# Performance work log

Hardware: AMD Instinct MI355X
Metric: run time of the kernel (lower is better)

The kernel has to match this reference:

```python
import jax, jax.numpy as jnp
import numpy as np

N_DIM = 512
HIDDEN = 512


def setup_inputs() -> dict:
    key = jax.random.key(0)
    ks = jax.random.split(key, 9)
    s = 0.02
    x = jax.random.normal(ks[0], (4, 4096, N_DIM), dtype=jnp.float32)
    Wq = jax.random.normal(ks[1], (N_DIM, HIDDEN), dtype=jnp.float32) * s
    bq = jnp.zeros((HIDDEN,), dtype=jnp.float32)
    Wk = jax.random.normal(ks[2], (N_DIM, HIDDEN), dtype=jnp.float32) * s
    bk = jnp.zeros((HIDDEN,), dtype=jnp.float32)
    Wv = jax.random.normal(ks[3], (N_DIM, HIDDEN), dtype=jnp.float32) * s
    bv = jnp.zeros((HIDDEN,), dtype=jnp.float32)
    Wo = jax.random.normal(ks[4], (HIDDEN, N_DIM), dtype=jnp.float32) * s
    bo = jnp.zeros((N_DIM,), dtype=jnp.float32)
    return {"x": x, "Wq": Wq, "bq": bq, "Wk": Wk, "bk": bk,
            "Wv": Wv, "bv": bv, "Wo": Wo, "bo": bo}


def reference(x, Wq, bq, Wk, bk, Wv, bv, Wo, bo):
    # x: [B, S, n_dim]
    q = jnp.einsum('bsd,dh->bsh', x, Wq) + bq  # [B,S,H]
    k = jnp.einsum('bsd,dh->bsh', x, Wk) + bk
    v = jnp.einsum('bsd,dh->bsh', x, Wv) + bv
    # NOTE: original module uses UNSCALED scores (no 1/sqrt(d))
    scores = jnp.einsum('bqh,bkh->bqk', q, k)  # [B,S,S]
    attn = jax.nn.softmax(scores, axis=-1)
    y = jnp.einsum('bqk,bkh->bqh', attn, v)
    return jnp.einsum('bsh,hd->bsd', y, Wo) + bo
```

## Files before the change

### kernel.cpp

```cpp
#include <hip/hip_runtime.h>
#include <hip/hip_bf16.h>

typedef _Float16 h8 __attribute__((ext_vector_type(8)));
typedef __bf16   b8 __attribute__((ext_vector_type(8)));
typedef float    f4 __attribute__((ext_vector_type(4)));

#define B_    4
#define S_    4096
#define D_    512
#define ROWS_ (B_ * S_)
#define NQKV_ 1536
#define BR    64
#define BC2   64
#define NIT2  (S_ / BC2)
#define KP3   520
#define KT3   (BC2 * KP3)
#define PP3   72
#define MSH   (30.0f * 1.4426950408889634f)
#define L2E   1.4426950408889634f

__device__ __forceinline__ void gl_lds16(const void* src, void* dst) {
    __builtin_amdgcn_global_load_lds(
        (const __attribute__((address_space(1))) unsigned int*)src,
        (__attribute__((address_space(3))) unsigned int*)dst, 16, 0, 0);
}

__global__ __launch_bounds__(256) void convert_all(
    const float* __restrict__ x,
    const float* __restrict__ Wq, const float* __restrict__ Wk, const float* __restrict__ Wv,
    const float* __restrict__ bq, const float* __restrict__ bk, const float* __restrict__ bv,
    const float* __restrict__ Wo,
    _Float16* __restrict__ xh, _Float16* __restrict__ wqkvT, _Float16* __restrict__ woT,
    float* __restrict__ bqkv)
{
    long i0 = (long)blockIdx.x * blockDim.x + threadIdx.x;
    long stride = (long)gridDim.x * blockDim.x;
    const long NX  = (long)ROWS_ * D_;
    const long NW  = (long)D_ * NQKV_;
    const long NWO = (long)D_ * D_;

    for (long i = i0; i < NX; i += stride) xh[i] = (_Float16)x[i];

    for (long i = i0; i < NW; i += stride) {
        long n = i >> 9, k = i & 511;
        long which = n >> 9, nn = n & 511;
        const float* W = (which == 0) ? Wq : (which == 1) ? Wk : Wv;
        wqkvT[i] = (_Float16)W[k * 512 + nn];
    }
    for (long i = i0; i < NWO; i += stride) {
        long n = i >> 9, k = i & 511;
        woT[i] = (_Float16)Wo[k * 512 + n];
    }
    for (long i = i0; i < NQKV_; i += stride) {
        long which = i >> 9, nn = i & 511;
        const float* bb = (which == 0) ? bq : (which == 1) ? bk : bv;
        bqkv[i] = bb[nn];
    }
}

template <bool OUT_F16>
__global__ __launch_bounds__(256) void gemm_bt(
    const _Float16* __restrict__ A, const _Float16* __restrict__ BT,
    const float* __restrict__ bias, void* __restrict__ Cout,
    int M, int N, int K, __bf16* __restrict__ vPout)
{
    __shared__ _Float16 As[128 * 32];
    __shared__ _Float16 Bs[128 * 32];

    int tid = threadIdx.x;
    int w = tid >> 6, lane = tid & 63, quad = lane >> 4, l16 = lane & 15;
    long row0 = (long)blockIdx.x * 128, col0 = (long)blockIdx.y * 128;
    int wr = (w >> 1) * 64, wc = (w & 1) * 64;

    f4 acc[4][4];
    for (int i = 0; i < 4; i++)
        for (int j = 0; j < 4; j++) acc[i][j] = (f4){0.f, 0.f, 0.f, 0.f};

    const int lrow = lane >> 2;
    const int lcol = (lane & 3) * 8;

    for (int k0 = 0; k0 < K; k0 += 32) {
        __syncthreads();
#pragma unroll
        for (int i = 0; i < 2; i++) {
            int seg = w * 2 + i;
            gl_lds16(A  + (row0 + seg * 16 + lrow) * K + k0 + lcol, As + seg * 512);
            gl_lds16(BT + (col0 + seg * 16 + lrow) * K + k0 + lcol, Bs + seg * 512);
        }
        __syncthreads();
        h8 af[4], bf[4];
        for (int i = 0; i < 4; i++) af[i] = *(const h8*)(As + (wr + i * 16 + l16) * 32 + quad * 8);
        for (int j = 0; j < 4; j++) bf[j] = *(const h8*)(Bs + (wc + j * 16 + l16) * 32 + quad * 8);
        for (int i = 0; i < 4; i++)
            for (int j = 0; j < 4; j++)
                acc[i][j] = __builtin_amdgcn_mfma_f32_16x16x32_f16(af[i], bf[j], acc[i][j], 0, 0, 0);
    }

    if (OUT_F16 && vPout != nullptr && col0 >= 1024) {
        for (int i = 0; i < 4; i++) {
            long row = row0 + wr + i * 16 + quad * 4;
            int bb   = (int)(row >> 12);
            int s    = (int)(row & 4095);
            int kt32 = s >> 5;
            int qq   = (s >> 3) & 3;
            int k3   = s & 7;
            for (int j = 0; j < 4; j++) {
                int dglob = (int)(col0 - 1024) + wc + j * 16;
                int dt = dglob >> 4;
                long off = (((long)bb * 128 + kt32) * 32 + dt) * 512
                         + (qq * 16 + l16) * 8 + k3;
                union { __bf16 h[4]; uint2 u2; } pk;
                for (int r = 0; r < 4; r++)
                    pk.h[r] = (__bf16)(acc[i][j][r] + bias[col0 + wc + j * 16 + l16]);
                *(uint2*)(vPout + off) = pk.u2;
            }
        }
    } else {
        for (int i = 0; i < 4; i++)
            for (int j = 0; j < 4; j++)
                for (int r = 0; r < 4; r++) {
                    long row = row0 + wr + i * 16 + quad * 4 + r;
                    long col = col0 + wc + j * 16 + l16;
                    float v = acc[i][j][r] + bias[col];
                    if (OUT_F16) ((_Float16*)Cout)[row * N + col] = (_Float16)v;
                    else         ((float*)Cout)[row * N + col]    = v;
                }
    }
}

__global__ __launch_bounds__(512, 2) void attn_kernel(const _Float16* __restrict__ qkv,
                                                      const __bf16* __restrict__ vP,
                                                      _Float16* __restrict__ yb)
{
    __shared__ _Float16 Ks[2 * KT3];
    __shared__ __bf16   Ps[2 * BR * PP3];
    __shared__ float    lpart[2][BR];

    const int tid = threadIdx.x;
    const int w = tid >> 6, lane = tid & 63, quad = lane >> 4, l16 = lane & 15;

    const int bid = blockIdx.x;
    const int xcd = bid & 7;
    const int b = xcd >> 1;
    const long q0 = (long)((xcd & 1) * 32 + (bid >> 3)) * BR;
    const long rowBase = (long)b * S_;

    const _Float16* kbase = qkv + rowBase * NQKV_ + 512;

#pragma unroll
    for (int i = 0; i < 8; i++) {
        int r = w * 8 + i;
        gl_lds16(kbase + (long)r * NQKV_ + lane * 8, Ks + r * KP3);
    }

    if (w < 4) {
        const int rs0 = (w & 1) * 32;
        const int kg0 = (w >> 1) * 32;

        h8 Qf0[16], Qf1[16];
        {
            const _Float16* q0p = qkv + (rowBase + q0 + rs0 + l16) * NQKV_;
            const _Float16* q1p = q0p + 16 * NQKV_;
#pragma unroll
            for (int ks = 0; ks < 16; ks++) {
                Qf0[ks] = *(const h8*)(q0p + ks * 32 + quad * 8);
                Qf1[ks] = *(const h8*)(q1p + ks * 32 + quad * 8);
            }
        }
        float lo0[4] = {0.f, 0.f, 0.f, 0.f};
        float lo1[4] = {0.f, 0.f, 0.f, 0.f};

        __syncthreads();

        for (int kt = 0; kt < NIT2; kt++) {
            if (kt + 1 < NIT2) {
                const _Float16* kn = kbase + (long)(kt + 1) * BC2 * NQKV_;
                _Float16* kd = Ks + ((kt + 1) & 1) * KT3;
#pragma unroll
                for (int i = 0; i < 8; i++) {
                    int r = w * 8 + i;
                    gl_lds16(kn + (long)r * NQKV_ + lane * 8, kd + r * KP3);
                }
            }
            f4 S[2][2][2];
#pragma unroll
            for (int a = 0; a < 2; a++)
#pragma unroll
                for (int c = 0; c < 2; c++)
#pragma unroll
                    for (int d = 0; d < 2; d++) S[a][c][d] = (f4){0.f, 0.f, 0.f, 0.f};
            const _Float16* kr0 = Ks + (kt & 1) * KT3 + (kg0 + l16) * KP3 + quad * 8;
            const _Float16* kr1 = kr0 + 16 * KP3;
            __builtin_amdgcn_s_setprio(1);
#pragma unroll
            for (int ks = 0; ks < 8; ks++) {
                h8 a0 = *(const h8*)(kr0 + ks * 32);
                h8 a1 = *(const h8*)(kr0 + (ks + 8) * 32);
                h8 c0 = *(const h8*)(kr1 + ks * 32);
                h8 c1 = *(const h8*)(kr1 + (ks + 8) * 32);
                S[0][0][0] = __builtin_amdgcn_mfma_f32_16x16x32_f16(Qf0[ks],     a0, S[0][0][0], 0, 0, 0);
                S[1][0][0] = __builtin_amdgcn_mfma_f32_16x16x32_f16(Qf1[ks],     a0, S[1][0][0], 0, 0, 0);
                S[0][1][0] = __builtin_amdgcn_mfma_f32_16x16x32_f16(Qf0[ks],     c0, S[0][1][0], 0, 0, 0);
                S[1][1][0] = __builtin_amdgcn_mfma_f32_16x16x32_f16(Qf1[ks],     c0, S[1][1][0], 0, 0, 0);
                S[0][0][1] = __builtin_amdgcn_mfma_f32_16x16x32_f16(Qf0[ks + 8], a1, S[0][0][1], 0, 0, 0);
                S[1][0][1] = __builtin_amdgcn_mfma_f32_16x16x32_f16(Qf1[ks + 8], a1, S[1][0][1], 0, 0, 0);
                S[0][1][1] = __builtin_amdgcn_mfma_f32_16x16x32_f16(Qf0[ks + 8], c1, S[0][1][1], 0, 0, 0);
                S[1][1][1] = __builtin_amdgcn_mfma_f32_16x16x32_f16(Qf1[ks + 8], c1, S[1][1][1], 0, 0, 0);
            }
            __builtin_amdgcn_s_setprio(0);
            __bf16* ps = Ps + (kt & 1) * (BR * PP3);
#pragma unroll
            for (int r = 0; r < 4; r++) {
                float p00 = exp2f((S[0][0][0][r] + S[0][0][1][r]) * L2E - MSH);
                float p01 = exp2f((S[0][1][0][r] + S[0][1][1][r]) * L2E - MSH);
                float p10 = exp2f((S[1][0][0][r] + S[1][0][1][r]) * L2E - MSH);
                float p11 = exp2f((S[1][1][0][r] + S[1][1][1][r]) * L2E - MSH);
                __bf16 b00 = (__bf16)p00, b01 = (__bf16)p01;
                __bf16 b10 = (__bf16)p10, b11 = (__bf16)p11;
                int r0 = (rs0 + quad * 4 + r) * PP3;
                int r1 = (rs0 + 16 + quad * 4 + r) * PP3;
                ps[r0 + kg0 + l16]      = b00;
                ps[r0 + kg0 + 16 + l16] = b01;
                ps[r1 + kg0 + l16]      = b10;
                ps[r1 + kg0 + 16 + l16] = b11;
                lo0[r] += (float)b00 + (float)b01;
                lo1[r] += (float)b10 + (float)b11;
            }
            __builtin_amdgcn_sched_barrier(0);
            asm volatile("s_waitcnt vmcnt(0)");
            asm volatile("s_waitcnt lgkmcnt(0)");
            __builtin_amdgcn_s_barrier();
            __builtin_amdgcn_sched_barrier(0);
        }

#pragma unroll
        for (int r = 0; r < 4; r++)
#pragma unroll
            for (int m = 1; m < 16; m <<= 1) {
                lo0[r] += __shfl_xor(lo0[r], m, 16);
                lo1[r] += __shfl_xor(lo1[r], m, 16);
            }
        if (l16 == 0)
            for (int r = 0; r < 4; r++) {
                lpart[w >> 1][rs0 + quad * 4 + r]      = lo0[r];
                lpart[w >> 1][rs0 + 16 + quad * 4 + r] = lo1[r];
            }
        __syncthreads();
    } else {
        const int cv = w - 4;
        const __bf16* vpbase = vP + ((long)b * 128 * 32 + cv * 8) * 512 + lane * 8;

        f4 O[4][8];
#pragma unroll
        for (int rt = 0; rt < 4; rt++)
#pragma unroll
            for (int ct = 0; ct < 8; ct++) O[rt][ct] = (f4){0.f, 0.f, 0.f, 0.f};
        b8 vreg[16];

        __syncthreads();

        for (int kt = 0; kt < NIT2; kt++) {
            if (kt + 1 < NIT2) {
                const _Float16* kn = kbase + (long)(kt + 1) * BC2 * NQKV_;
                _Float16* kd = Ks + ((kt + 1) & 1) * KT3;
#pragma unroll
                for (int i = 0; i < 8; i++) {
                    int r = w * 8 + i;
                    gl_lds16(kn + (long)r * NQKV_ + lane * 8, kd + r * KP3);
                }
            }
            __builtin_amdgcn_sched_barrier(0);
            if (kt > 0) {
                if (kt < NIT2 - 1) asm volatile("s_waitcnt vmcnt(8)");
                else               asm volatile("s_waitcnt vmcnt(0)");
                const __bf16* ps = Ps + ((kt - 1) & 1) * (BR * PP3);
                __builtin_amdgcn_s_setprio(1);
#pragma unroll
                for (int rt = 0; rt < 4; rt++) {
                    b8 pa0 = *(const b8*)(ps + (rt * 16 + l16) * PP3 + quad * 8);
                    b8 pa1 = *(const b8*)(ps + (rt * 16 + l16) * PP3 + 32 + quad * 8);
#pragma unroll
                    for (int ct = 0; ct < 8; ct++) {
                        O[rt][ct] = __builtin_amdgcn_mfma_f32_16x16x32_bf16(pa0, vreg[ct],     O[rt][ct], 0, 0, 0);
                        O[rt][ct] = __builtin_amdgcn_mfma_f32_16x16x32_bf16(pa1, vreg[8 + ct], O[rt][ct], 0, 0, 0);
                    }
                }
                __builtin_amdgcn_s_setprio(0);
            }
            {
                const __bf16* vs0 = vpbase + (long)(2 * kt) * (32 * 512);
#pragma unroll
                for (int ct = 0; ct < 8; ct++) {
                    vreg[ct]     = *(const b8*)(vs0 + ct * 512);
                    vreg[8 + ct] = *(const b8*)(vs0 + 32 * 512 + ct * 512);
                }
            }
            __builtin_amdgcn_sched_barrier(0);
            asm volatile("s_waitcnt vmcnt(16)");
            asm volatile("s_waitcnt lgkmcnt(0)");
            __builtin_amdgcn_s_barrier();
            __builtin_amdgcn_sched_barrier(0);
        }
        asm volatile("s_waitcnt vmcnt(0)");
        {
            const __bf16* ps = Ps + ((NIT2 - 1) & 1) * (BR * PP3);
#pragma unroll
            for (int rt = 0; rt < 4; rt++) {
                b8 pa0 = *(const b8*)(ps + (rt * 16 + l16) * PP3 + quad * 8);
                b8 pa1 = *(const b8*)(ps + (rt * 16 + l16) * PP3 + 32 + quad * 8);
#pragma unroll
                for (int ct = 0; ct < 8; ct++) {
                    O[rt][ct] = __builtin_amdgcn_mfma_f32_16x16x32_bf16(pa0, vreg[ct],     O[rt][ct], 0, 0, 0);
                    O[rt][ct] = __builtin_amdgcn_mfma_f32_16x16x32_bf16(pa1, vreg[8 + ct], O[rt][ct], 0, 0, 0);
                }
            }
        }
        __syncthreads();

#pragma unroll
        for (int rt = 0; rt < 4; rt++) {
            f4 l0 = *(const f4*)(&lpart[0][rt * 16 + quad * 4]);
            f4 l1 = *(const f4*)(&lpart[1][rt * 16 + quad * 4]);
            float li[4];
            for (int r = 0; r < 4; r++) li[r] = 1.f / (l0[r] + l1[r]);
            for (int ct = 0; ct < 8; ct++)
                for (int r = 0; r < 4; r++) {
                    long row = rowBase + q0 + rt * 16 + quad * 4 + r;
                    long col = cv * 128 + ct * 16 + l16;
                    yb[row * 512 + col] = (_Float16)(O[rt][ct][r] * li[r]);
                }
        }
    }
}

extern "C" void kernel_launch(void* const* d_in, const int* in_sizes, int n_in,
                              void* d_out, int out_size, void* d_ws, size_t ws_size,
                              hipStream_t stream)
{
    const float* x  = (const float*)d_in[0];
    const float* Wq = (const float*)d_in[1];
    const float* bq = (const float*)d_in[2];
    const float* Wk = (const float*)d_in[3];
    const float* bk = (const float*)d_in[4];
    const float* Wv = (const float*)d_in[5];
    const float* bv = (const float*)d_in[6];
    const float* Wo = (const float*)d_in[7];
    const float* bo = (const float*)d_in[8];
    float* out = (float*)d_out;

    char* ws = (char*)d_ws;
    _Float16* xh    = (_Float16*)(ws);
    _Float16* qkv   = (_Float16*)(ws + 16777216);
    __bf16*   vP    = (__bf16*)(ws + 67108864);
    _Float16* yb    = (_Float16*)(ws + 83886080);
    _Float16* wqkvT = (_Float16*)(ws + 100663296);
    _Float16* woT   = (_Float16*)(ws + 102236160);
    float*    bqkv  = (float*)(ws + 102760448);

    convert_all<<<2048, 256, 0, stream>>>(x, Wq, Wk, Wv, bq, bk, bv, Wo,
                                          xh, wqkvT, woT, bqkv);

    dim3 g1(128, 12);
    gemm_bt<true><<<g1, 256, 0, stream>>>(xh, wqkvT, bqkv, qkv, ROWS_, NQKV_, D_, vP);

    attn_kernel<<<256, 512, 0, stream>>>(qkv, vP, yb);

    dim3 g2(128, 4);
    gemm_bt<false><<<g2, 256, 0, stream>>>(yb, woT, bo, out, ROWS_, D_, D_, nullptr);
}
```

Measured before the change: 308.9 us.

## Double wavefronts per block in attention and GEMM kernels

The attention kernel goes from 512 to 1024 threads: eight score waves each own 16 query rows, and eight PV waves each own 64 output columns. This halves per-wave register state (Q fragments, O accumulators, V registers) and spreads the same per-block work over more waves. The GEMM kernel moves to 512 threads with 128x256 tiles, so each A tile is reused across more columns and the grid is half as large. In exchange, 1024-thread blocks allow fewer resident blocks per CU, and the register budget per thread drops, which risks spilling.

```diff
diff --git a/kernel.cpp b/kernel.cpp
--- a/kernel.cpp
+++ b/kernel.cpp
@@ -59,18 +59,18 @@
 }
 
 template <bool OUT_F16>
-__global__ __launch_bounds__(256) void gemm_bt(
+__global__ __launch_bounds__(512) void gemm_bt(
     const _Float16* __restrict__ A, const _Float16* __restrict__ BT,
     const float* __restrict__ bias, void* __restrict__ Cout,
     int M, int N, int K, __bf16* __restrict__ vPout)
 {
     __shared__ _Float16 As[128 * 32];
-    __shared__ _Float16 Bs[128 * 32];
+    __shared__ _Float16 Bs[256 * 32];
 
     int tid = threadIdx.x;
     int w = tid >> 6, lane = tid & 63, quad = lane >> 4, l16 = lane & 15;
-    long row0 = (long)blockIdx.x * 128, col0 = (long)blockIdx.y * 128;
-    int wr = (w >> 1) * 64, wc = (w & 1) * 64;
+    long row0 = (long)blockIdx.x * 128, col0 = (long)blockIdx.y * 256;
+    int wr = (w >> 2) * 64, wc = (w & 3) * 64;
 
     f4 acc[4][4];
     for (int i = 0; i < 4; i++)
@@ -81,12 +81,9 @@
 
     for (int k0 = 0; k0 < K; k0 += 32) {
         __syncthreads();
-#pragma unroll
-        for (int i = 0; i < 2; i++) {
-            int seg = w * 2 + i;
-            gl_lds16(A  + (row0 + seg * 16 + lrow) * K + k0 + lcol, As + seg * 512);
-            gl_lds16(BT + (col0 + seg * 16 + lrow) * K + k0 + lcol, Bs + seg * 512);
-        }
+        gl_lds16(A  + (row0 + w * 16 + lrow) * K + k0 + lcol,        As + w * 512);
+        gl_lds16(BT + (col0 + w * 16 + lrow) * K + k0 + lcol,        Bs + w * 512);
+        gl_lds16(BT + (col0 + (w + 8) * 16 + lrow) * K + k0 + lcol,  Bs + (w + 8) * 512);
         __syncthreads();
         h8 af[4], bf[4];
         for (int i = 0; i < 4; i++) af[i] = *(const h8*)(As + (wr + i * 16 + l16) * 32 + quad * 8);
@@ -128,9 +125,9 @@
     }
 }
 
-__global__ __launch_bounds__(512, 2) void attn_kernel(const _Float16* __restrict__ qkv,
-                                                      const __bf16* __restrict__ vP,
-                                                      _Float16* __restrict__ yb)
+__global__ __launch_bounds__(1024) void attn_kernel(const _Float16* __restrict__ qkv,
+                                                    const __bf16* __restrict__ vP,
+                                                    _Float16* __restrict__ yb)
 {
     __shared__ _Float16 Ks[2 * KT3];
     __shared__ __bf16   Ps[2 * BR * PP3];
@@ -148,27 +145,23 @@
     const _Float16* kbase = qkv + rowBase * NQKV_ + 512;
 
 #pragma unroll
-    for (int i = 0; i < 8; i++) {
-        int r = w * 8 + i;
+    for (int i = 0; i < 4; i++) {
+        int r = w * 4 + i;
         gl_lds16(kbase + (long)r * NQKV_ + lane * 8, Ks + r * KP3);
     }
 
-    if (w < 4) {
-        const int rs0 = (w & 1) * 32;
-        const int kg0 = (w >> 1) * 32;
-
-        h8 Qf0[16], Qf1[16];
+    if (w < 8) {
+        const int rs0 = (w & 3) * 16;
+        const int kg0 = (w >> 2) * 32;
+
+        h8 Qf[16];
         {
-            const _Float16* q0p = qkv + (rowBase + q0 + rs0 + l16) * NQKV_;
-            const _Float16* q1p = q0p + 16 * NQKV_;
-#pragma unroll
-            for (int ks = 0; ks < 16; ks++) {
-                Qf0[ks] = *(const h8*)(q0p + ks * 32 + quad * 8);
-                Qf1[ks] = *(const h8*)(q1p + ks * 32 + quad * 8);
-            }
-        }
-        float lo0[4] = {0.f, 0.f, 0.f, 0.f};
-        float lo1[4] = {0.f, 0.f, 0.f, 0.f};
+            const _Float16* qp = qkv + (rowBase + q0 + rs0 + l16) * NQKV_;
+#pragma unroll
+            for (int ks = 0; ks < 16; ks++)
+                Qf[ks] = *(const h8*)(qp + ks * 32 + quad * 8);
+        }
+        float lo[4] = {0.f, 0.f, 0.f, 0.f};
 
         __syncthreads();
 
@@ -177,18 +170,13 @@
                 const _Float16* kn = kbase + (long)(kt + 1) * BC2 * NQKV_;
                 _Float16* kd = Ks + ((kt + 1) & 1) * KT3;
 #pragma unroll
-                for (int i = 0; i < 8; i++) {
-                    int r = w * 8 + i;
+                for (int i = 0; i < 4; i++) {
+                    int r = w * 4 + i;
                     gl_lds16(kn + (long)r * NQKV_ + lane * 8, kd + r * KP3);
                 }
             }
-            f4 S[2][2][2];
-#pragma unroll
-            for (int a = 0; a < 2; a++)
-#pragma unroll
-                for (int c = 0; c < 2; c++)
-#pragma unroll
-                    for (int d = 0; d < 2; d++) S[a][c][d] = (f4){0.f, 0.f, 0.f, 0.f};
+            f4 S00 = (f4){0.f,0.f,0.f,0.f}, S01 = (f4){0.f,0.f,0.f,0.f};
+            f4 S10 = (f4){0.f,0.f,0.f,0.f}, S11 = (f4){0.f,0.f,0.f,0.f};
             const _Float16* kr0 = Ks + (kt & 1) * KT3 + (kg0 + l16) * KP3 + quad * 8;
             const _Float16* kr1 = kr0 + 16 * KP3;
             __builtin_amdgcn_s_setprio(1);
@@ -198,33 +186,22 @@
                 h8 a1 = *(const h8*)(kr0 + (ks + 8) * 32);
                 h8 c0 = *(const h8*)(kr1 + ks * 32);
                 h8 c1 = *(const h8*)(kr1 + (ks + 8) * 32);
-                S[0][0][0] = __builtin_amdgcn_mfma_f32_16x16x32_f16(Qf0[ks],     a0, S[0][0][0], 0, 0, 0);
-                S[1][0][0] = __builtin_amdgcn_mfma_f32_16x16x32_f16(Qf1[ks],     a0, S[1][0][0], 0, 0, 0);
-                S[0][1][0] = __builtin_amdgcn_mfma_f32_16x16x32_f16(Qf0[ks],     c0, S[0][1][0], 0, 0, 0);
-                S[1][1][0] = __builtin_amdgcn_mfma_f32_16x16x32_f16(Qf1[ks],     c0, S[1][1][0], 0, 0, 0);
-                S[0][0][1] = __builtin_amdgcn_mfma_f32_16x16x32_f16(Qf0[ks + 8], a1, S[0][0][1], 0, 0, 0);
-                S[1][0][1] = __builtin_amdgcn_mfma_f32_16x16x32_f16(Qf1[ks + 8], a1, S[1][0][1], 0, 0, 0);
-                S[0][1][1] = __builtin_amdgcn_mfma_f32_16x16x32_f16(Qf0[ks + 8], c1, S[0][1][1], 0, 0, 0);
-                S[1][1][1] = __builtin_amdgcn_mfma_f32_16x16x32_f16(Qf1[ks + 8], c1, S[1][1][1], 0, 0, 0);
+                S00 = __builtin_amdgcn_mfma_f32_16x16x32_f16(Qf[ks],     a0, S00, 0, 0, 0);
+                S10 = __builtin_amdgcn_mfma_f32_16x16x32_f16(Qf[ks],     c0, S10, 0, 0, 0);
+                S01 = __builtin_amdgcn_mfma_f32_16x16x32_f16(Qf[ks + 8], a1, S01, 0, 0, 0);
+                S11 = __builtin_amdgcn_mfma_f32_16x16x32_f16(Qf[ks + 8], c1, S11, 0, 0, 0);
             }
             __builtin_amdgcn_s_setprio(0);
             __bf16* ps = Ps + (kt & 1) * (BR * PP3);
 #pragma unroll
             for (int r = 0; r < 4; r++) {
-                float p00 = exp2f((S[0][0][0][r] + S[0][0][1][r]) * L2E - MSH);
-                float p01 = exp2f((S[0][1][0][r] + S[0][1][1][r]) * L2E - MSH);
-                float p10 = exp2f((S[1][0][0][r] + S[1][0][1][r]) * L2E - MSH);
-                float p11 = exp2f((S[1][1][0][r] + S[1][1][1][r]) * L2E - MSH);
-                __bf16 b00 = (__bf16)p00, b01 = (__bf16)p01;
-                __bf16 b10 = (__bf16)p10, b11 = (__bf16)p11;
-                int r0 = (rs0 + quad * 4 + r) * PP3;
-                int r1 = (rs0 + 16 + quad * 4 + r) * PP3;
-                ps[r0 + kg0 + l16]      = b00;
-                ps[r0 + kg0 + 16 + l16] = b01;
-                ps[r1 + kg0 + l16]      = b10;
-                ps[r1 + kg0 + 16 + l16] = b11;
-                lo0[r] += (float)b00 + (float)b01;
-                lo1[r] += (float)b10 + (float)b11;
+                float p0 = exp2f((S00[r] + S01[r]) * L2E - MSH);
+                float p1 = exp2f((S10[r] + S11[r]) * L2E - MSH);
+                __bf16 b0 = (__bf16)p0, b1 = (__bf16)p1;
+                int rr = (rs0 + quad * 4 + r) * PP3;
+                ps[rr + kg0 + l16]      = b0;
+                ps[rr + kg0 + 16 + l16] = b1;
+                lo[r] += (float)b0 + (float)b1;
             }
             __builtin_amdgcn_sched_barrier(0);
             asm volatile("s_waitcnt vmcnt(0)");
@@ -236,26 +213,22 @@
 #pragma unroll
         for (int r = 0; r < 4; r++)
 #pragma unroll
-            for (int m = 1; m < 16; m <<= 1) {
-                lo0[r] += __shfl_xor(lo0[r], m, 16);
-                lo1[r] += __shfl_xor(lo1[r], m, 16);
-            }
+            for (int m = 1; m < 16; m <<= 1)
+                lo[r] += __shfl_xor(lo[r], m, 16);
         if (l16 == 0)
-            for (int r = 0; r < 4; r++) {
-                lpart[w >> 1][rs0 + quad * 4 + r]      = lo0[r];
-                lpart[w >> 1][rs0 + 16 + quad * 4 + r] = lo1[r];
-            }
+            for (int r = 0; r < 4; r++)
+                lpart[w >> 2][rs0 + quad * 4 + r] = lo[r];
         __syncthreads();
     } else {
-        const int cv = w - 4;
-        const __bf16* vpbase = vP + ((long)b * 128 * 32 + cv * 8) * 512 + lane * 8;
-
-        f4 O[4][8];
+        const int cv = w - 8;
+        const __bf16* vpbase = vP + ((long)b * 128 * 32 + cv * 4) * 512 + lane * 8;
+
+        f4 O[4][4];
 #pragma unroll
         for (int rt = 0; rt < 4; rt++)
 #pragma unroll
-            for (int ct = 0; ct < 8; ct++) O[rt][ct] = (f4){0.f, 0.f, 0.f, 0.f};
-        b8 vreg[16];
+            for (int ct = 0; ct < 4; ct++) O[rt][ct] = (f4){0.f, 0.f, 0.f, 0.f};
+        b8 vreg[8];
 
         __syncthreads();
 
@@ -264,14 +237,14 @@
                 const _Float16* kn = kbase + (long)(kt + 1) * BC2 * NQKV_;
                 _Float16* kd = Ks + ((kt + 1) & 1) * KT3;
 #pragma unroll
-                for (int i = 0; i < 8; i++) {
-                    int r = w * 8 + i;
+                for (int i = 0; i < 4; i++) {
+                    int r = w * 4 + i;
                     gl_lds16(kn + (long)r * NQKV_ + lane * 8, kd + r * KP3);
                 }
             }
             __builtin_amdgcn_sched_barrier(0);
             if (kt > 0) {
-                if (kt < NIT2 - 1) asm volatile("s_waitcnt vmcnt(8)");
+                if (kt < NIT2 - 1) asm volatile("s_waitcnt vmcnt(4)");
                 else               asm volatile("s_waitcnt vmcnt(0)");
                 const __bf16* ps = Ps + ((kt - 1) & 1) * (BR * PP3);
                 __builtin_amdgcn_s_setprio(1);
@@ -280,23 +253,23 @@
                     b8 pa0 = *(const b8*)(ps + (rt * 16 + l16) * PP3 + quad * 8);
                     b8 pa1 = *(const b8*)(ps + (rt * 16 + l16) * PP3 + 32 + quad * 8);
 #pragma unroll
-                    for (int ct = 0; ct < 8; ct++) {
+                    for (int ct = 0; ct < 4; ct++) {
                         O[rt][ct] = __builtin_amdgcn_mfma_f32_16x16x32_bf16(pa0, vreg[ct],     O[rt][ct], 0, 0, 0);
-                        O[rt][ct] = __builtin_amdgcn_mfma_f32_16x16x32_bf16(pa1, vreg[8 + ct], O[rt][ct], 0, 0, 0);
+                        O[rt][ct] = __builtin_amdgcn_mfma_f32_16x16x32_bf16(pa1, vreg[4 + ct], O[rt][ct], 0, 0, 0);
                     }
                 }
                 __builtin_amdgcn_s_setprio(0);
             }
             {
-                const __bf16* vs0 = vpbase + (long)(2 * kt) * (32 * 512);
-#pragma unroll
-                for (int ct = 0; ct < 8; ct++) {
-                    vreg[ct]     = *(const b8*)(vs0 + ct * 512);
-                    vreg[8 + ct] = *(const b8*)(vs0 + 32 * 512 + ct * 512);
-                }
-            }
-            __builtin_amdgcn_sched_barrier(0);
-            asm volatile("s_waitcnt vmcnt(16)");
+                const __bf16* vs = vpbase + (long)(2 * kt) * (32 * 512);
+#pragma unroll
+                for (int ct = 0; ct < 4; ct++) {
+                    vreg[ct]     = *(const b8*)(vs + ct * 512);
+                    vreg[4 + ct] = *(const b8*)(vs + 32 * 512 + ct * 512);
+                }
+            }
+            __builtin_amdgcn_sched_barrier(0);
+            asm volatile("s_waitcnt vmcnt(8)");
             asm volatile("s_waitcnt lgkmcnt(0)");
             __builtin_amdgcn_s_barrier();
             __builtin_amdgcn_sched_barrier(0);
@@ -309,9 +282,9 @@
                 b8 pa0 = *(const b8*)(ps + (rt * 16 + l16) * PP3 + quad * 8);
                 b8 pa1 = *(const b8*)(ps + (rt * 16 + l16) * PP3 + 32 + quad * 8);
 #pragma unroll
-                for (int ct = 0; ct < 8; ct++) {
+                for (int ct = 0; ct < 4; ct++) {
                     O[rt][ct] = __builtin_amdgcn_mfma_f32_16x16x32_bf16(pa0, vreg[ct],     O[rt][ct], 0, 0, 0);
-                    O[rt][ct] = __builtin_amdgcn_mfma_f32_16x16x32_bf16(pa1, vreg[8 + ct], O[rt][ct], 0, 0, 0);
+                    O[rt][ct] = __builtin_amdgcn_mfma_f32_16x16x32_bf16(pa1, vreg[4 + ct], O[rt][ct], 0, 0, 0);
                 }
             }
         }
@@ -323,10 +296,10 @@
             f4 l1 = *(const f4*)(&lpart[1][rt * 16 + quad * 4]);
             float li[4];
             for (int r = 0; r < 4; r++) li[r] = 1.f / (l0[r] + l1[r]);
-            for (int ct = 0; ct < 8; ct++)
+            for (int ct = 0; ct < 4; ct++)
                 for (int r = 0; r < 4; r++) {
                     long row = rowBase + q0 + rt * 16 + quad * 4 + r;
-                    long col = cv * 128 + ct * 16 + l16;
+                    long col = cv * 64 + ct * 16 + l16;
                     yb[row * 512 + col] = (_Float16)(O[rt][ct][r] * li[r]);
                 }
         }
@@ -360,11 +333,11 @@
     convert_all<<<2048, 256, 0, stream>>>(x, Wq, Wk, Wv, bq, bk, bv, Wo,
                                           xh, wqkvT, woT, bqkv);
 
-    dim3 g1(128, 12);
-    gemm_bt<true><<<g1, 256, 0, stream>>>(xh, wqkvT, bqkv, qkv, ROWS_, NQKV_, D_, vP);
-
-    attn_kernel<<<256, 512, 0, stream>>>(qkv, vP, yb);
-
-    dim3 g2(128, 4);
-    gemm_bt<false><<<g2, 256, 0, stream>>>(yb, woT, bo, out, ROWS_, D_, D_, nullptr);
-}
+    dim3 g1(128, 6);
+    gemm_bt<true><<<g1, 512, 0, stream>>>(xh, wqkvT, bqkv, qkv, ROWS_, NQKV_, D_, vP);
+
+    attn_kernel<<<256, 1024, 0, stream>>>(qkv, vP, yb);
+
+    dim3 g2(128, 2);
+    gemm_bt<false><<<g2, 512, 0, stream>>>(yb, woT, bo, out, ROWS_, D_, D_, nullptr);
+}
```

Result: no change. 309.7 us (+0.3%).

## Double-buffer GEMM LDS tiles and widen block to 128x256 with 512 threads

Applied to the files above, without the earlier changes.

Projection GEMMs now use a two-stage LDS double buffer, so the next K-slice is prefetched with global_load_lds while MFMAs run on the current slice, with one barrier per iteration instead of two. Block tile grows to 128x256 with 8 waves, halving the grid in the N dimension so each A tile is reused by more waves. This uses more LDS per block and may reduce occupancy. The GEMMs are a small part of total time next to the attention kernel.

```diff
diff --git a/kernel.cpp b/kernel.cpp
--- a/kernel.cpp
+++ b/kernel.cpp
@@ -59,18 +59,18 @@
 }
 
 template <bool OUT_F16>
-__global__ __launch_bounds__(256) void gemm_bt(
+__global__ __launch_bounds__(512) void gemm_bt(
     const _Float16* __restrict__ A, const _Float16* __restrict__ BT,
     const float* __restrict__ bias, void* __restrict__ Cout,
     int M, int N, int K, __bf16* __restrict__ vPout)
 {
-    __shared__ _Float16 As[128 * 32];
-    __shared__ _Float16 Bs[128 * 32];
+    __shared__ _Float16 As[2][128 * 32];
+    __shared__ _Float16 Bs[2][256 * 32];
 
     int tid = threadIdx.x;
     int w = tid >> 6, lane = tid & 63, quad = lane >> 4, l16 = lane & 15;
-    long row0 = (long)blockIdx.x * 128, col0 = (long)blockIdx.y * 128;
-    int wr = (w >> 1) * 64, wc = (w & 1) * 64;
+    long row0 = (long)blockIdx.x * 128, col0 = (long)blockIdx.y * 256;
+    int wr = (w >> 2) * 64, wc = (w & 3) * 64;
 
     f4 acc[4][4];
     for (int i = 0; i < 4; i++)
@@ -78,22 +78,32 @@
 
     const int lrow = lane >> 2;
     const int lcol = (lane & 3) * 8;
-
-    for (int k0 = 0; k0 < K; k0 += 32) {
-        __syncthreads();
-#pragma unroll
-        for (int i = 0; i < 2; i++) {
-            int seg = w * 2 + i;
-            gl_lds16(A  + (row0 + seg * 16 + lrow) * K + k0 + lcol, As + seg * 512);
-            gl_lds16(BT + (col0 + seg * 16 + lrow) * K + k0 + lcol, Bs + seg * 512);
-        }
-        __syncthreads();
+    const int NT = K >> 5;
+
+    gl_lds16(A  + (row0 + w * 16 + lrow) * K + lcol,        As[0] + w * 512);
+    gl_lds16(BT + (col0 + w * 16 + lrow) * K + lcol,        Bs[0] + w * 512);
+    gl_lds16(BT + (col0 + (w + 8) * 16 + lrow) * K + lcol,  Bs[0] + (w + 8) * 512);
+    __syncthreads();
+
+    for (int t = 0; t < NT; ++t) {
+        const int cur = t & 1;
+        if (t + 1 < NT) {
+            const int k1 = (t + 1) * 32;
+            gl_lds16(A  + (row0 + w * 16 + lrow) * K + k1 + lcol,        As[cur ^ 1] + w * 512);
+            gl_lds16(BT + (col0 + w * 16 + lrow) * K + k1 + lcol,        Bs[cur ^ 1] + w * 512);
+            gl_lds16(BT + (col0 + (w + 8) * 16 + lrow) * K + k1 + lcol,  Bs[cur ^ 1] + (w + 8) * 512);
+        }
         h8 af[4], bf[4];
-        for (int i = 0; i < 4; i++) af[i] = *(const h8*)(As + (wr + i * 16 + l16) * 32 + quad * 8);
-        for (int j = 0; j < 4; j++) bf[j] = *(const h8*)(Bs + (wc + j * 16 + l16) * 32 + quad * 8);
+        for (int i = 0; i < 4; i++) af[i] = *(const h8*)(As[cur] + (wr + i * 16 + l16) * 32 + quad * 8);
+        for (int j = 0; j < 4; j++) bf[j] = *(const h8*)(Bs[cur] + (wc + j * 16 + l16) * 32 + quad * 8);
         for (int i = 0; i < 4; i++)
             for (int j = 0; j < 4; j++)
                 acc[i][j] = __builtin_amdgcn_mfma_f32_16x16x32_f16(af[i], bf[j], acc[i][j], 0, 0, 0);
+        __builtin_amdgcn_sched_barrier(0);
+        asm volatile("s_waitcnt vmcnt(0)");
+        asm volatile("s_waitcnt lgkmcnt(0)");
+        __builtin_amdgcn_s_barrier();
+        __builtin_amdgcn_sched_barrier(0);
     }
 
     if (OUT_F16 && vPout != nullptr && col0 >= 1024) {
@@ -360,11 +370,11 @@
     convert_all<<<2048, 256, 0, stream>>>(x, Wq, Wk, Wv, bq, bk, bv, Wo,
                                           xh, wqkvT, woT, bqkv);
 
-    dim3 g1(128, 12);
-    gemm_bt<true><<<g1, 256, 0, stream>>>(xh, wqkvT, bqkv, qkv, ROWS_, NQKV_, D_, vP);
+    dim3 g1(128, 6);
+    gemm_bt<true><<<g1, 512, 0, stream>>>(xh, wqkvT, bqkv, qkv, ROWS_, NQKV_, D_, vP);
 
     attn_kernel<<<256, 512, 0, stream>>>(qkv, vP, yb);
 
-    dim3 g2(128, 4);
-    gemm_bt<false><<<g2, 256, 0, stream>>>(yb, woT, bo, out, ROWS_, D_, D_, nullptr);
-}
+    dim3 g2(128, 2);
+    gemm_bt<false><<<g2, 512, 0, stream>>>(yb, woT, bo, out, ROWS_, D_, D_, nullptr);
+}
```

Result: no change. 313.5 us (+1.5%).
